# Kernel optimization log

Hardware: AMD Instinct MI355X
Metric: run time of the kernel (lower is better)

The kernel has to match this reference:

```python
import jax, jax.numpy as jnp
import numpy as np

HEADS = 16
DIM_HEAD = 64
LN_EPS = 1e-5


def rotate_half(t):
    # '... (j d) -> ... j d' with j=2, then cat(-x2, x1)
    d = t.shape[-1] // 2
    t1, t2 = t[..., :d], t[..., d:]
    return jnp.concatenate([-t2, t1], axis=-1)


def apply_rotary_pos_emb(t, pos):
    # t: (BT, h, L, dh); pos: (L, rotate_dim)
    rd = pos.shape[-1]
    pos = pos[None, None]  # (1, 1, L, rd)
    t_rot, t_pass = t[..., :rd], t[..., rd:]
    t_rot = t_rot * jnp.cos(pos) + rotate_half(t_rot) * jnp.sin(pos)
    return jnp.concatenate([t_rot, t_pass], axis=-1)


def setup_inputs() -> dict:
    key = jax.random.key(0)
    ks = jax.random.split(key, 4)
    B, T, L, D = 2, 8, 1024, 1024
    inner = HEADS * DIM_HEAD
    x = jax.random.normal(ks[0], (B, T * L, D), dtype=jnp.float32)
    gamma = jnp.ones((D,), jnp.float32)
    beta = jnp.zeros((D,), jnp.float32)
    W_qkv = jax.random.normal(ks[1], (D, 3 * inner), jnp.float32) * (D ** -0.5)
    b_qkv = jnp.zeros((3 * inner,), jnp.float32)
    W_out = jax.random.normal(ks[2], (inner, D), jnp.float32) * (inner ** -0.5)
    # standard GPT-NeoX-style rope angles for the spatial axis, rotate_dim=32
    rot_dim = 32
    inv_freq = 1.0 / (10000.0 ** (jnp.arange(0, rot_dim, 2, dtype=jnp.float32) / rot_dim))
    freqs = jnp.arange(L, dtype=jnp.float32)[:, None] * inv_freq[None, :]  # (L, 16)
    rotary_pos_emb = jnp.concatenate([freqs, freqs], axis=-1)  # (L, 32)
    return {"x": x, "gamma": gamma, "beta": beta, "W_qkv": W_qkv,
            "b_qkv": b_qkv, "W_out": W_out, "rotary_pos_emb": rotary_pos_emb,
            "T": T, "L": L}


def reference(x, gamma, beta, W_qkv, b_qkv, W_out, rotary_pos_emb, T, L):
    B, _, D = x.shape
    h, dh = HEADS, DIM_HEAD
    scale = dh ** -0.5
    # LayerNorm
    mean = jnp.mean(x, axis=-1, keepdims=True)
    var = jnp.mean(jnp.square(x - mean), axis=-1, keepdims=True)
    xn = (x - mean) * jax.lax.rsqrt(var + LN_EPS) * gamma + beta
    # (B, T*L, D) -> (B*T, L, D)
    xr = xn.reshape(B * T, L, D)
    qkv = xr @ W_qkv + b_qkv  # (BT, L, 3*h*dh)
    q, k, v = jnp.split(qkv, 3, axis=-1)
    def to_heads(t):
        return t.reshape(B * T, L, h, dh).transpose(0, 2, 1, 3)  # (BT, h, L, dh)
    q, k, v = map(to_heads, (q, k, v))
    q = apply_rotary_pos_emb(q, rotary_pos_emb)
    k = apply_rotary_pos_emb(k, rotary_pos_emb)
    sim = jnp.einsum('bhid,bhjd->bhij', q, k) * scale
    attn = jax.nn.softmax(sim.astype(jnp.float32), axis=-1).astype(q.dtype)
    out = jnp.einsum('bhij,bhjd->bhid', attn, v)  # (BT, h, L, dh)
    out = out.transpose(0, 2, 1, 3).reshape(B * T, L, h * dh)
    out = out @ W_out  # (BT, L, D)
    return out.reshape(B, T * L, D)
```

## Files before the change

### kernel.cpp

```cpp
#include <hip/hip_runtime.h>
#include <hip/hip_bf16.h>
#include <stdint.h>

typedef short bf16x8 __attribute__((ext_vector_type(8)));
typedef float f32x4  __attribute__((ext_vector_type(4)));
typedef unsigned short u16x4 __attribute__((ext_vector_type(4)));
typedef unsigned int   u32x2 __attribute__((ext_vector_type(2)));

#define DEV __device__ __forceinline__

DEV ushort f2bf(float f){
  unsigned u = __float_as_uint(f);
  u += 0x7FFFu + ((u >> 16) & 1u);
  return (ushort)(u >> 16);
}

DEV unsigned pack_bf16x2(float lo, float hi){
  __hip_bfloat162 r = __float22bfloat162_rn(float2{lo, hi});
  return *(unsigned*)&r;
}

DEV void async16(const void* g, void* l){
  __builtin_amdgcn_global_load_lds((const __attribute__((address_space(1))) void*)g,
                                   (__attribute__((address_space(3))) void*)l, 16, 0, 0);
}

__global__ __launch_bounds__(256) void preproc_kernel(
    const float* __restrict__ x, const float* __restrict__ gamma,
    const float* __restrict__ beta, ushort* __restrict__ xn,
    const float* __restrict__ Wqkv, ushort* __restrict__ Wqt,
    const float* __restrict__ Wout, ushort* __restrict__ Wot,
    const float* __restrict__ rope, float2* __restrict__ cst)
{
  __shared__ __align__(16) ushort tile[64][65];
  __shared__ float red[8];
  const int b = blockIdx.x, t = threadIdx.x;
  if (b < 16384) {
    const float4* xr = (const float4*)(x + (size_t)b * 1024);
    float4 v = xr[t];
    float s  = v.x + v.y + v.z + v.w;
    float s2 = v.x*v.x + v.y*v.y + v.z*v.z + v.w*v.w;
    #pragma unroll
    for (int o = 1; o < 64; o <<= 1) { s += __shfl_xor(s, o); s2 += __shfl_xor(s2, o); }
    int lane = t & 63, wv = t >> 6;
    if (lane == 0) { red[wv] = s; red[4 + wv] = s2; }
    __syncthreads();
    s  = red[0] + red[1] + red[2] + red[3];
    s2 = red[4] + red[5] + red[6] + red[7];
    float mean = s * (1.0f / 1024.0f);
    float var  = s2 * (1.0f / 1024.0f) - mean * mean;
    float rs = rsqrtf(var + 1e-5f);
    float4 g = ((const float4*)gamma)[t], bb = ((const float4*)beta)[t];
    u16x4 o4;
    o4[0] = f2bf((v.x - mean) * rs * g.x + bb.x);
    o4[1] = f2bf((v.y - mean) * rs * g.y + bb.y);
    o4[2] = f2bf((v.z - mean) * rs * g.z + bb.z);
    o4[3] = f2bf((v.w - mean) * rs * g.w + bb.w);
    ((u16x4*)(xn + (size_t)b * 1024))[t] = o4;
  } else if (b < 17408) {
    const float* A; ushort* At; int R, C, c0, r0;
    if (b < 17152) { int bb2 = b - 16384; A = Wqkv; At = Wqt; R = 1024; C = 3072;
                     c0 = (bb2 % 48) * 64; r0 = (bb2 / 48) * 64; }
    else           { int bb2 = b - 17152; A = Wout; At = Wot; R = 1024; C = 1024;
                     c0 = (bb2 % 16) * 64; r0 = (bb2 / 16) * 64; }
    int tx = t & 63, ty = t >> 6;
    #pragma unroll
    for (int i = 0; i < 64; i += 4)
      tile[ty + i][tx] = f2bf(A[(size_t)(r0 + ty + i) * C + c0 + tx]);
    __syncthreads();
    #pragma unroll
    for (int i = 0; i < 64; i += 4)
      At[(size_t)(c0 + ty + i) * R + r0 + tx] = tile[tx][ty + i];
  } else {
    int i = (b - 17408) * 256 + t;
    int l = i >> 4, d = i & 15;
    float p = rope[l * 32 + d];
    float s, c;
    sincosf(p, &s, &c);
    cst[i] = float2{c, s};
  }
}

template<bool OUT_BF16, bool HAS_BIAS, bool ROPE>
__global__ __launch_bounds__(512, 2) void gemm256_kernel(
    const ushort* __restrict__ A, const ushort* __restrict__ Bt,
    const float* __restrict__ bias, void* __restrict__ Cout,
    const float2* __restrict__ cst,
    int M, int Nrow, int K)
{
  __shared__ __align__(16) ushort As[2][2][256][32];
  __shared__ __align__(16) ushort Bs[2][2][256][32];
  const int tid = threadIdx.x, lane = tid & 63, w = tid >> 6;
  const int fr = lane & 15, fg = lane >> 4;
  const int wr = w >> 2, wc = w & 3;

  int i  = blockIdx.x & 255;
  int r  = blockIdx.x >> 8;
  int il = (i & 7) * 32 + (i >> 3);
  int bx = r * 4 + (il & 3);
  int by = il >> 2;
  const int aRow0 = by * 256, bCol0 = bx * 256;
  const size_t ldb = (size_t)K * 2;

  const int lrow = lane >> 2, lch = lane & 3;
  const int g0 = w * 2, g1 = w * 2 + 1;
  const int r0 = g0 * 16 + lrow, r1 = g1 * 16 + lrow;
  const int sc0 = ((lch ^ ((r0 & 3) ^ ((r0 >> 2) & 3))) << 4);
  const int sc1 = ((lch ^ ((r1 & 3) ^ ((r1 >> 2) & 3))) << 4);
  const char* Ab = (const char*)A + (size_t)aRow0 * ldb;
  const char* Bb = (const char*)Bt + (size_t)bCol0 * ldb;
  const size_t ga0 = (size_t)r0 * ldb, ga1 = (size_t)r1 * ldb;
  char* ldsA = (char*)&As[0][0][0][0];
  char* ldsB = (char*)&Bs[0][0][0][0];
  const int ld0 = g0 * 1024, ld1 = g1 * 1024;

  int rbA[8], rbB[4];
  #pragma unroll
  for (int mf = 0; mf < 8; ++mf) {
    int rr = wr * 128 + mf * 16 + fr;
    rbA[mf] = rr * 64 + ((fg ^ ((rr & 3) ^ ((rr >> 2) & 3))) << 4);
  }
  #pragma unroll
  for (int nf = 0; nf < 4; ++nf) {
    int rr = wc * 64 + nf * 16 + fr;
    rbB[nf] = rr * 64 + ((fg ^ ((rr & 3) ^ ((rr >> 2) & 3))) << 4);
  }

  f32x4 acc[8][4];
  f32x4 z = {0.f, 0.f, 0.f, 0.f};
  #pragma unroll
  for (int mf = 0; mf < 8; ++mf)
    #pragma unroll
    for (int nf = 0; nf < 4; ++nf) acc[mf][nf] = z;

  auto stage = [&](int buf, int kt, int kc) {
    const char* ak = Ab + (size_t)kt * 128 + kc * 64;
    const char* bk = Bb + (size_t)kt * 128 + kc * 64;
    int lo = buf * 32768 + kc * 16384;
    async16(ak + ga0 + sc0, ldsA + lo + ld0);
    async16(ak + ga1 + sc1, ldsA + lo + ld1);
    async16(bk + ga0 + sc0, ldsB + lo + ld0);
    async16(bk + ga1 + sc1, ldsB + lo + ld1);
  };

  stage(0, 0, 0);
  stage(0, 0, 1);
  asm volatile("s_waitcnt vmcnt(4)" ::: "memory");
  __builtin_amdgcn_s_barrier();

  const int nk = K >> 6;
  for (int kt = 0; kt < nk; ++kt) {
    int buf = kt & 1;
    bool pre = (kt + 1 < nk);
    #pragma unroll
    for (int kc = 0; kc < 2; ++kc) {
      const char* ab = ldsA + buf * 32768 + kc * 16384;
      const char* bb = ldsB + buf * 32768 + kc * 16384;
      bf16x8 a[8], b[4];
      #pragma unroll
      for (int mf = 0; mf < 8; ++mf) a[mf] = *(const bf16x8*)(ab + rbA[mf]);
      #pragma unroll
      for (int nf = 0; nf < 4; ++nf) b[nf] = *(const bf16x8*)(bb + rbB[nf]);
      if (pre) stage(buf ^ 1, kt + 1, kc);
      __builtin_amdgcn_s_setprio(1);
      #pragma unroll
      for (int mf = 0; mf < 8; ++mf)
        #pragma unroll
        for (int nf = 0; nf < 4; ++nf)
          acc[mf][nf] = __builtin_amdgcn_mfma_f32_16x16x32_bf16(a[mf], b[nf], acc[mf][nf], 0, 0, 0);
      __builtin_amdgcn_s_setprio(0);
      if (pre) { asm volatile("s_waitcnt vmcnt(4)" ::: "memory"); }
      else     { asm volatile("s_waitcnt vmcnt(0)" ::: "memory"); }
      __builtin_amdgcn_s_barrier();
    }
  }

  #pragma unroll
  for (int pr = 0; pr < 2; ++pr) {
    int nf0 = pr * 2, nf1 = nf0 + 1;
    int gc0 = bCol0 + wc * 64 + nf0 * 16 + fr;
    int gc1 = gc0 + 16;
    float bv0 = HAS_BIAS ? bias[gc0] : 0.0f;
    float bv1 = HAS_BIAS ? bias[gc1] : 0.0f;
    bool rot = ROPE && (pr == 0) && (gc0 < 2048);
    float qs = (ROPE && gc0 < 1024) ? 0.18033688f : 1.0f;
    #pragma unroll
    for (int mf = 0; mf < 8; ++mf) {
      int gr0 = aRow0 + wr * 128 + mf * 16 + fg * 4;
      #pragma unroll
      for (int rr2 = 0; rr2 < 4; ++rr2) {
        int gr = gr0 + rr2;
        float a = acc[mf][nf0][rr2] + bv0;
        float b = acc[mf][nf1][rr2] + bv1;
        if (rot) {
          int l = gr & 1023;
          float2 cp = cst[l * 16 + fr];
          float an = fmaf(a, cp.x, -b * cp.y);
          b = fmaf(b, cp.x, a * cp.y);
          a = an;
        }
        a *= qs; b *= qs;
        if (OUT_BF16) {
          ((ushort*)Cout)[(size_t)gr * Nrow + gc0] = f2bf(a);
          ((ushort*)Cout)[(size_t)gr * Nrow + gc1] = f2bf(b);
        } else {
          ((float*)Cout)[(size_t)gr * Nrow + gc0] = a;
          ((float*)Cout)[(size_t)gr * Nrow + gc1] = b;
        }
      }
    }
  }
}

__global__ __launch_bounds__(256) void vtrans_kernel(const ushort* __restrict__ qkv,
                                                     ushort* __restrict__ vT)
{
  __shared__ __align__(16) ushort tile[64][65];
  int bh = blockIdx.x & 255, lt = blockIdx.x >> 8;
  int bt = bh >> 4, h = bh & 15;
  int tx = threadIdx.x & 63, ty = threadIdx.x >> 6;
  const ushort* src = qkv + (size_t)(bt * 1024 + lt * 64) * 3072 + 2048 + h * 64;
  #pragma unroll
  for (int i = 0; i < 64; i += 4)
    tile[ty + i][tx] = src[(size_t)(ty + i) * 3072 + tx];
  __syncthreads();
  ushort* dst = vT + (size_t)bh * 64 * 1024 + lt * 64;
  #pragma unroll
  for (int i = 0; i < 64; i += 4)
    dst[(size_t)(ty + i) * 1024 + tx] = tile[tx][ty + i];
}

__global__ __launch_bounds__(256, 3) void attn_kernel(
    const ushort* __restrict__ qkv, const ushort* __restrict__ vT,
    ushort* __restrict__ aout)
{
  __shared__ __align__(16) ushort Ks[2][64 * 64];
  __shared__ __align__(16) ushort Vs[2][64 * 64];
  __shared__ __align__(16) ushort Ps[4][32 * 64];
  const int tid = threadIdx.x, lane = tid & 63, w = tid >> 6;
  const int fr = lane & 15, fg = lane >> 4;
  const int bh = blockIdx.x & 255, qt = blockIdx.x >> 8;
  const int bt = bh >> 4, h = bh & 15;
  const size_t ld = 3072;
  const ushort* qbase = qkv + (size_t)bt * 1024 * ld + h * 64;
  const ushort* kbase = qbase + 1024;
  const ushort* vtb = vT + (size_t)bh * 64 * 1024;
  const int srow = lane >> 3;
  const int scol = (((lane & 7) ^ srow) << 4);
  const int swz = (fr & 7) << 4;

  bf16x8 ones;
  #pragma unroll
  for (int j = 0; j < 8; ++j) ones[j] = (short)0x3F80;

  bf16x8 qfr[2][2];
  #pragma unroll
  for (int qf = 0; qf < 2; ++qf)
    #pragma unroll
    for (int kc = 0; kc < 2; ++kc) {
      int qrow = qt * 128 + w * 32 + qf * 16 + fr;
      qfr[qf][kc] = *(const bf16x8*)((const char*)(qbase + (size_t)qrow * ld) + kc * 64 + fg * 16);
    }

  f32x4 o[2][4], ls[2];
  f32x4 z = {0.f, 0.f, 0.f, 0.f};
  #pragma unroll
  for (int a = 0; a < 2; ++a) {
    ls[a] = z;
    #pragma unroll
    for (int b = 0; b < 4; ++b) o[a][b] = z;
  }
  float m_[2] = {-1e30f, -1e30f};

  auto stage = [&](int buf, int t) {
    #pragma unroll
    for (int i = 0; i < 2; ++i) {
      int ch = w * 2 + i;
      async16((const char*)(kbase + (size_t)(t * 64 + ch * 8 + srow) * ld) + scol,
              (char*)Ks[buf] + ch * 1024);
      async16((const char*)(vtb + (size_t)(ch * 8 + srow) * 1024) + t * 128 + scol,
              (char*)Vs[buf] + ch * 1024);
    }
  };

  stage(0, 0);
  __syncthreads();
  for (int t = 0; t < 16; ++t) {
    int cur = t & 1;
    if (t + 1 < 16) stage(cur ^ 1, t + 1);

    bf16x8 kf[4][2];
    #pragma unroll
    for (int kvf = 0; kvf < 4; ++kvf)
      #pragma unroll
      for (int kc = 0; kc < 2; ++kc)
        kf[kvf][kc] = *(const bf16x8*)((const char*)Ks[cur] + (kvf * 16 + fr) * 128 +
                                       ((kc * 64 + fg * 16) ^ swz));
    float alpha[2] = {1.0f, 1.0f};
    int   need[2];
    #pragma unroll
    for (int qf = 0; qf < 2; ++qf) {
      f32x4 st[4];
      #pragma unroll
      for (int kvf = 0; kvf < 4; ++kvf) st[kvf] = z;
      __builtin_amdgcn_s_setprio(1);
      #pragma unroll
      for (int kc = 0; kc < 2; ++kc)
        #pragma unroll
        for (int kvf = 0; kvf < 4; ++kvf)
          st[kvf] = __builtin_amdgcn_mfma_f32_16x16x32_bf16(kf[kvf][kc], qfr[qf][kc], st[kvf], 0, 0, 0);
      __builtin_amdgcn_s_setprio(0);
      float mx = -1e30f;
      #pragma unroll
      for (int kvf = 0; kvf < 4; ++kvf)
        #pragma unroll
        for (int r = 0; r < 4; ++r) mx = fmaxf(mx, st[kvf][r]);
      mx = fmaxf(mx, __shfl_xor(mx, 16));
      mx = fmaxf(mx, __shfl_xor(mx, 32));
      need[qf] = __any(mx > m_[qf] + 11.53f);
      if (need[qf]) {
        float mn = fmaxf(m_[qf], mx);
        alpha[qf] = __builtin_amdgcn_exp2f(m_[qf] - mn);
        m_[qf] = mn;
      }
      float mb = m_[qf];
      int qrow = qf * 16 + fr;
      #pragma unroll
      for (int kvf = 0; kvf < 4; ++kvf) {
        float p0 = __builtin_amdgcn_exp2f(st[kvf][0] - mb);
        float p1 = __builtin_amdgcn_exp2f(st[kvf][1] - mb);
        float p2 = __builtin_amdgcn_exp2f(st[kvf][2] - mb);
        float p3 = __builtin_amdgcn_exp2f(st[kvf][3] - mb);
        u32x2 u;
        u[0] = pack_bf16x2(p0, p1);
        u[1] = pack_bf16x2(p2, p3);
        *(u32x2*)((char*)Ps[w] + qrow * 128 + ((kvf * 32 + fg * 8) ^ swz)) = u;
      }
    }
    #pragma unroll
    for (int of = 0; of < 2; ++of) {
      if (need[of]) {
        float ar[4];
        #pragma unroll
        for (int r = 0; r < 4; ++r) ar[r] = __shfl(alpha[of], fg * 4 + r);
        #pragma unroll
        for (int cf = 0; cf < 4; ++cf)
          #pragma unroll
          for (int r = 0; r < 4; ++r) o[of][cf][r] *= ar[r];
        #pragma unroll
        for (int r = 0; r < 4; ++r) ls[of][r] *= ar[r];
      }
    }
    __builtin_amdgcn_s_setprio(1);
    #pragma unroll
    for (int kc4 = 0; kc4 < 2; ++kc4) {
      bf16x8 pa[2];
      #pragma unroll
      for (int of = 0; of < 2; ++of)
        pa[of] = *(const bf16x8*)((const char*)Ps[w] + (of * 16 + fr) * 128 +
                                  ((kc4 * 64 + fg * 16) ^ swz));
      #pragma unroll
      for (int cf = 0; cf < 4; ++cf) {
        bf16x8 vb = *(const bf16x8*)((const char*)Vs[cur] + (cf * 16 + fr) * 128 +
                                     ((kc4 * 64 + fg * 16) ^ swz));
        #pragma unroll
        for (int of = 0; of < 2; ++of)
          o[of][cf] = __builtin_amdgcn_mfma_f32_16x16x32_bf16(pa[of], vb, o[of][cf], 0, 0, 0);
      }
      #pragma unroll
      for (int of = 0; of < 2; ++of)
        ls[of] = __builtin_amdgcn_mfma_f32_16x16x32_bf16(pa[of], ones, ls[of], 0, 0, 0);
    }
    __builtin_amdgcn_s_setprio(0);
    __syncthreads();
  }
  #pragma unroll
  for (int of = 0; of < 2; ++of) {
    #pragma unroll
    for (int cf = 0; cf < 4; ++cf)
      #pragma unroll
      for (int r = 0; r < 4; ++r) {
        int grow_ = bt * 1024 + qt * 128 + w * 32 + of * 16 + fg * 4 + r;
        int gcol  = h * 64 + cf * 16 + fr;
        aout[(size_t)grow_ * 1024 + gcol] = f2bf(o[of][cf][r] / ls[of][r]);
      }
  }
}

extern "C" void kernel_launch(void* const* d_in, const int* in_sizes, int n_in,
                              void* d_out, int out_size, void* d_ws, size_t ws_size,
                              hipStream_t stream)
{
  const float* x     = (const float*)d_in[0];
  const float* gamma = (const float*)d_in[1];
  const float* beta  = (const float*)d_in[2];
  const float* Wqkv  = (const float*)d_in[3];
  const float* bqkv  = (const float*)d_in[4];
  const float* Wout  = (const float*)d_in[5];
  const float* rope  = (const float*)d_in[6];

  char* ws = (char*)d_ws;
  ushort* xn   = (ushort*)(ws + 0);
  ushort* qkvb = (ushort*)(ws + 33554432ULL);
  ushort* vT   = (ushort*)(ws + 134217728ULL);
  ushort* Wqt  = (ushort*)(ws + 167772160ULL);
  ushort* Wot  = (ushort*)(ws + 174063616ULL);
  float2* cst  = (float2*)(ws + 176160768ULL);
  ushort* aout = xn;

  preproc_kernel<<<17472, 256, 0, stream>>>(x, gamma, beta, xn,
                                            Wqkv, Wqt, Wout, Wot, rope, cst);
  gemm256_kernel<true, true, true><<<768, 512, 0, stream>>>(
      xn, Wqt, bqkv, (void*)qkvb, cst, 16384, 3072, 1024);
  vtrans_kernel<<<4096, 256, 0, stream>>>(qkvb, vT);
  attn_kernel<<<2048, 256, 0, stream>>>(qkvb, vT, aout);
  gemm256_kernel<false, false, false><<<256, 512, 0, stream>>>(
      aout, Wot, nullptr, d_out, nullptr, 16384, 1024, 1024);
}
```

Before: 317.9 us.

## Pass softmax probabilities through cross-lane shuffles instead of LDS, raise occupancy

Removes the per-wave P staging buffer in shared memory. The packed bf16 probabilities now stay in registers and are rearranged into the MFMA A-operand layout with __shfl and lane selects. This drops LDS writes and reads per tile and cuts shared memory per block, and the launch bound minimum blocks per CU goes from 3 to 4. In exchange it adds 16 shuffles per kc4 step (ds_bpermute, which still goes through the LDS hardware) and may put pressure on registers under the tighter occupancy bound.

```diff
diff --git a/kernel.cpp b/kernel.cpp
--- a/kernel.cpp
+++ b/kernel.cpp
@@ -230,13 +230,12 @@
     dst[(size_t)(ty + i) * 1024 + tx] = tile[tx][ty + i];
 }
 
-__global__ __launch_bounds__(256, 3) void attn_kernel(
+__global__ __launch_bounds__(256, 4) void attn_kernel(
     const ushort* __restrict__ qkv, const ushort* __restrict__ vT,
     ushort* __restrict__ aout)
 {
   __shared__ __align__(16) ushort Ks[2][64 * 64];
   __shared__ __align__(16) ushort Vs[2][64 * 64];
-  __shared__ __align__(16) ushort Ps[4][32 * 64];
   const int tid = threadIdx.x, lane = tid & 63, w = tid >> 6;
   const int fr = lane & 15, fg = lane >> 4;
   const int bh = blockIdx.x & 255, qt = blockIdx.x >> 8;
@@ -248,6 +247,9 @@
   const int srow = lane >> 3;
   const int scol = (((lane & 7) ^ srow) << 4);
   const int swz = (fr & 7) << 4;
+  const int slo = fr + ((fg & 1) << 5);
+  const int shi = slo + 16;
+  const bool hsel = (fg >> 1) != 0;
 
   bf16x8 ones;
   #pragma unroll
@@ -298,6 +300,7 @@
                                        ((kc * 64 + fg * 16) ^ swz));
     float alpha[2] = {1.0f, 1.0f};
     int   need[2];
+    unsigned pkv[2][4][2];
     #pragma unroll
     for (int qf = 0; qf < 2; ++qf) {
       f32x4 st[4];
@@ -324,17 +327,14 @@
         m_[qf] = mn;
       }
       float mb = m_[qf];
-      int qrow = qf * 16 + fr;
       #pragma unroll
       for (int kvf = 0; kvf < 4; ++kvf) {
         float p0 = __builtin_amdgcn_exp2f(st[kvf][0] - mb);
         float p1 = __builtin_amdgcn_exp2f(st[kvf][1] - mb);
         float p2 = __builtin_amdgcn_exp2f(st[kvf][2] - mb);
         float p3 = __builtin_amdgcn_exp2f(st[kvf][3] - mb);
-        u32x2 u;
-        u[0] = pack_bf16x2(p0, p1);
-        u[1] = pack_bf16x2(p2, p3);
-        *(u32x2*)((char*)Ps[w] + qrow * 128 + ((kvf * 32 + fg * 8) ^ swz)) = u;
+        pkv[qf][kvf][0] = pack_bf16x2(p0, p1);
+        pkv[qf][kvf][1] = pack_bf16x2(p2, p3);
       }
     }
     #pragma unroll
@@ -356,9 +356,23 @@
     for (int kc4 = 0; kc4 < 2; ++kc4) {
       bf16x8 pa[2];
       #pragma unroll
-      for (int of = 0; of < 2; ++of)
-        pa[of] = *(const bf16x8*)((const char*)Ps[w] + (of * 16 + fr) * 128 +
-                                  ((kc4 * 64 + fg * 16) ^ swz));
+      for (int of = 0; of < 2; ++of) {
+        unsigned wa, wb;
+        unsigned wd[4];
+        wa = (unsigned)__shfl((int)pkv[of][2 * kc4][0], slo);
+        wb = (unsigned)__shfl((int)pkv[of][2 * kc4 + 1][0], slo);
+        wd[0] = hsel ? wb : wa;
+        wa = (unsigned)__shfl((int)pkv[of][2 * kc4][1], slo);
+        wb = (unsigned)__shfl((int)pkv[of][2 * kc4 + 1][1], slo);
+        wd[1] = hsel ? wb : wa;
+        wa = (unsigned)__shfl((int)pkv[of][2 * kc4][0], shi);
+        wb = (unsigned)__shfl((int)pkv[of][2 * kc4 + 1][0], shi);
+        wd[2] = hsel ? wb : wa;
+        wa = (unsigned)__shfl((int)pkv[of][2 * kc4][1], shi);
+        wb = (unsigned)__shfl((int)pkv[of][2 * kc4 + 1][1], shi);
+        wd[3] = hsel ? wb : wa;
+        pa[of] = *(const bf16x8*)wd;
+      }
       #pragma unroll
       for (int cf = 0; cf < 4; ++cf) {
         bf16x8 vb = *(const bf16x8*)((const char*)Vs[cur] + (cf * 16 + fr) * 128 +
```

Result: slower. 350.2 us (+10.1%).
